# Kernel tuning notes

Hardware: AMD Instinct MI355X
Metric: run time of the kernel (lower is better)

The kernel has to match this reference:

```python
import jax, jax.numpy as jnp
import numpy as np

DIM = 128
CODEBOOK_SIZE = 1024


def setup_inputs() -> dict:
    key = jax.random.key(0)
    kx, ke = jax.random.split(key)
    x = jax.random.normal(kx, (16, 4096, DIM), dtype=jnp.float32)
    # kaiming_uniform_ on (codebook_size, dim): bound = sqrt(6 / fan_in), fan_in = dim
    bound = float(np.sqrt(6.0 / DIM))
    embed = jax.random.uniform(ke, (CODEBOOK_SIZE, DIM), dtype=jnp.float32,
                               minval=-bound, maxval=bound)
    return {"x": x, "embed": embed}


def reference(x, embed):
    orig_shape = x.shape
    flat = x.reshape(-1, x.shape[-1])                     # [N, D]
    x2 = jnp.sum(flat * flat, axis=1, keepdims=True)      # [N, 1]
    e2 = jnp.sum(embed * embed, axis=1)                   # [K]
    dist = -(x2 - 2.0 * (flat @ embed.T) + e2[None, :])   # [N, K]
    embed_ind = jnp.argmax(dist, axis=-1)                 # [N]
    embed_ind = embed_ind.reshape(orig_shape[:-1])        # [B, S]
    quantize = jnp.take(embed, embed_ind, axis=0)         # [B, S, D]
    return quantize, embed_ind
```

## Files before the change

### kernel.cpp

```cpp
#include <hip/hip_runtime.h>

#define DIM     128
#define NCODES  1024
#define TILE_M  64
#define BSTR    272
#define FLAGThr 0.018f
#define RPB     4
#define RGRID   1024

typedef __attribute__((ext_vector_type(8))) _Float16 half8;
typedef __attribute__((ext_vector_type(4))) _Float16 half4;
typedef __attribute__((ext_vector_type(4))) float    f32x4;


__global__ __launch_bounds__(256) void setup_kernel(
    const float* __restrict__ embed, double* __restrict__ e2d,
    float* __restrict__ e2f, _Float16* __restrict__ eh,
    float* __restrict__ embedT, int* __restrict__ cnt)
{
  __shared__ float tile[64][132];
  __shared__ double psum[4][64];
  if (blockIdx.x == 0 && threadIdx.x == 0) *cnt = 0;
  const int c0 = blockIdx.x * 64;
  const int t  = threadIdx.x;

  const f32x4* E4 = (const f32x4*)(embed + (size_t)c0 * DIM);
  #pragma unroll
  for (int i = 0; i < 8; ++i) {
    int e = t + i * 256;
    int r = e >> 5, c4 = e & 31;
    f32x4 v = E4[e];
    *(f32x4*)&tile[r][c4 * 4] = v;
    half4 h;
    h[0] = (_Float16)v[0]; h[1] = (_Float16)v[1];
    h[2] = (_Float16)v[2]; h[3] = (_Float16)v[3];
    *(half4*)&eh[(size_t)(c0 + r) * DIM + c4 * 4] = h;
  }
  __syncthreads();

  {
    int r = t & 63, part = t >> 6;
    double s = 0.0;
    #pragma unroll
    for (int k = 0; k < 32; ++k) {
      float v = tile[r][part * 32 + k];
      s += (double)v * v;
    }
    psum[part][r] = s;
  }
  __syncthreads();
  if (t < 64) {
    double s = psum[0][t] + psum[1][t] + psum[2][t] + psum[3][t];
    e2d[c0 + t] = s;
    e2f[c0 + t] = (float)s;
  }

  #pragma unroll
  for (int i = 0; i < 32; ++i) {
    int idx = t + i * 256;
    int k = idx >> 6, c = idx & 63;
    embedT[(size_t)k * NCODES + c0 + c] = tile[c][k];
  }
}

__global__ __launch_bounds__(256, 2) void pass1_kernel(
    const float* __restrict__ x, const float* __restrict__ embed,
    const _Float16* __restrict__ eh, const float* __restrict__ e2f,
    float* __restrict__ outQ, float* __restrict__ outIdx,
    int* __restrict__ cnt, int* __restrict__ list)
{
  __shared__ __align__(16) unsigned char lds[256 * BSTR];
  __shared__ float rb_best[4][TILE_M];
  __shared__ float rb_sec [4][TILE_M];
  __shared__ int   fidx[TILE_M];

  const int tid  = threadIdx.x;
  const int row0 = blockIdx.x * TILE_M;
  _Float16* xh = (_Float16*)lds;

  {
    const f32x4* x4 = (const f32x4*)(x + (size_t)row0 * DIM);
    #pragma unroll
    for (int i = 0; i < 8; ++i) {
      int e = tid + i * 256;
      int r = e >> 5, c4 = e & 31;
      f32x4 v = x4[e];
      half4 h;
      h[0] = (_Float16)v[0]; h[1] = (_Float16)v[1];
      h[2] = (_Float16)v[2]; h[3] = (_Float16)v[3];
      *(half4*)&xh[r * 136 + c4 * 4] = h;
    }
  }
  __syncthreads();

  const int l  = tid & 63, w = tid >> 6;
  const int rl = l & 15,  q = l >> 4;
  const int col0 = q * 8;

  half8 afrag[4][4];
  #pragma unroll
  for (int m = 0; m < 4; ++m)
    #pragma unroll
    for (int ks = 0; ks < 4; ++ks)
      afrag[m][ks] = *(const half8*)&xh[(m * 16 + rl) * 136 + ks * 32 + col0];

  float bestp[16], secp[16];
  #pragma unroll
  for (int s = 0; s < 16; ++s) { bestp[s] = -3.0e38f; secp[s] = -3.3e38f; }

  f32x4 t0[16];
  {
    const f32x4* src = (const f32x4*)eh;
    #pragma unroll
    for (int i = 0; i < 16; ++i) t0[i] = src[tid + i * 256];
  }
  __syncthreads();

  #pragma unroll
  for (int st = 0; st < 4; ++st) {
    #pragma unroll
    for (int i = 0; i < 16; ++i) {
      int e = tid + i * 256;
      *(f32x4*)&lds[(e >> 4) * BSTR + (e & 15) * 16] = t0[i];
    }
    f32x4 t1[16];
    if (st < 3) {
      const f32x4* src = (const f32x4*)(eh + (size_t)(st + 1) * 256 * DIM);
      #pragma unroll
      for (int i = 0; i < 16; ++i) t1[i] = src[tid + i * 256];
    }
    float vinit[4];
    #pragma unroll
    for (int sub = 0; sub < 4; ++sub)
      vinit[sub] = fmaf(-0.5f, e2f[st * 256 + w * 64 + sub * 16 + rl], -16.0f);

    __syncthreads();

    #pragma unroll
    for (int sub = 0; sub < 4; ++sub) {
      const int codeL  = w * 64 + sub * 16 + rl;
      const int mycode = st * 256 + codeL;
      half8 bfrag[4];
      #pragma unroll
      for (int ks = 0; ks < 4; ++ks)
        bfrag[ks] = *(const half8*)&lds[codeL * BSTR + ks * 64 + q * 16];
      f32x4 acc[4];
      #pragma unroll
      for (int m = 0; m < 4; ++m)
        acc[m] = (f32x4){vinit[sub], vinit[sub], vinit[sub], vinit[sub]};
      #pragma unroll
      for (int ks = 0; ks < 4; ++ks)
        #pragma unroll
        for (int m = 0; m < 4; ++m)
          acc[m] = __builtin_amdgcn_mfma_f32_16x16x32_f16(afrag[m][ks], bfrag[ks], acc[m], 0, 0, 0);
      #pragma unroll
      for (int m = 0; m < 4; ++m)
        #pragma unroll
        for (int r = 0; r < 4; ++r) {
          const int s = m * 4 + r;
          float scp = __int_as_float((__float_as_int(acc[m][r]) & ~1023) | mycode);
          secp[s]  = __builtin_amdgcn_fmed3f(scp, bestp[s], secp[s]);
          bestp[s] = fmaxf(bestp[s], scp);
        }
    }
    if (st < 3) {
      __syncthreads();
      #pragma unroll
      for (int i = 0; i < 16; ++i) t0[i] = t1[i];
    }
  }

  #pragma unroll
  for (int off = 1; off < 16; off <<= 1) {
    #pragma unroll
    for (int s = 0; s < 16; ++s) {
      float ob = __shfl_xor(bestp[s], off, 16);
      float os = __shfl_xor(secp[s],  off, 16);
      secp[s]  = fmaxf(__builtin_amdgcn_fmed3f(bestp[s], ob, secp[s]), os);
      bestp[s] = fmaxf(bestp[s], ob);
    }
  }
  if (rl == 0) {
    #pragma unroll
    for (int m = 0; m < 4; ++m)
      #pragma unroll
      for (int r = 0; r < 4; ++r) {
        int s = m * 4 + r;
        int row = m * 16 + q * 4 + r;
        rb_best[w][row] = bestp[s];
        rb_sec [w][row] = secp[s];
      }
  }
  __syncthreads();

  if (tid < TILE_M) {
    float bv = rb_best[0][tid], sv = rb_sec[0][tid];
    #pragma unroll
    for (int ww = 1; ww < 4; ++ww) {
      float ob = rb_best[ww][tid], os = rb_sec[ww][tid];
      sv = fmaxf(__builtin_amdgcn_fmed3f(bv, ob, sv), os);
      bv = fmaxf(bv, ob);
    }
    int bi = __float_as_int(bv) & 1023;
    int grow = row0 + tid;
    outIdx[grow] = (float)bi;
    fidx[tid] = bi;
    if (bv - sv <= FLAGThr) {
      int p = atomicAdd(cnt, 1);
      list[p] = grow;
    }
  }
  __syncthreads();

  {
    const f32x4* E4   = (const f32x4*)embed;
    f32x4*       out4 = (f32x4*)(outQ + (size_t)row0 * DIM);
    #pragma unroll
    for (int i = 0; i < 8; ++i) {
      int e = tid + i * 256;
      int r = e >> 5, c4 = e & 31;
      out4[e] = E4[fidx[r] * 32 + c4];
    }
  }
}

__global__ __launch_bounds__(256) void refine2_kernel(
    const float* __restrict__ x, const float* __restrict__ embed,
    const float* __restrict__ embedT,
    const double* __restrict__ e2d, const float* __restrict__ e2f,
    float* __restrict__ outQ, float* __restrict__ outIdx,
    const int* __restrict__ cnt, const int* __restrict__ list)
{
  __shared__ f32x4 xst[DIM];
  __shared__ float rb1[RPB][4], rb2[RPB][4];
  __shared__ int   ri1[RPB][4], ri2[RPB][4];
  __shared__ int   cand[RPB][2];

  const int t = threadIdx.x;
  const int l = t & 63, w = t >> 6;
  const int n = *cnt;
  float* xsf = (float*)xst;

  for (int base = blockIdx.x * RPB; base < n; base += RGRID * RPB) {
    const int nr = min(RPB, n - base);
    #pragma unroll
    for (int i = 0; i < 2; ++i) {
      int idx = t + i * 256;
      int r = idx >> 7, k = idx & 127;
      float v = 0.f;
      if (r < nr) v = x[(size_t)list[base + r] * DIM + k];
      xsf[k * RPB + r] = v;
    }
    __syncthreads();

    f32x4 dot[RPB];
    #pragma unroll
    for (int r = 0; r < RPB; ++r) dot[r] = (f32x4){0.f, 0.f, 0.f, 0.f};
    const f32x4* eT4 = (const f32x4*)embedT;
    #pragma unroll 4
    for (int k = 0; k < DIM; ++k) {
      f32x4 e4  = eT4[k * 256 + t];
      f32x4 xk4 = xst[k];
      #pragma unroll
      for (int r = 0; r < RPB; ++r) {
        dot[r][0] = fmaf(xk4[r], e4[0], dot[r][0]);
        dot[r][1] = fmaf(xk4[r], e4[1], dot[r][1]);
        dot[r][2] = fmaf(xk4[r], e4[2], dot[r][2]);
        dot[r][3] = fmaf(xk4[r], e4[3], dot[r][3]);
      }
    }

    #pragma unroll
    for (int r = 0; r < RPB; ++r) {
      float b1 = 3.4e38f, b2 = 3.4e38f; int i1 = 0, i2 = 0;
      #pragma unroll
      for (int j = 0; j < 4; ++j) {
        int c = 4 * t + j;
        float sc = fmaf(-2.0f, dot[r][j], e2f[c]);
        bool better = (sc < b1);
        float lv = better ? b1 : sc;  int li = better ? i1 : c;
        if (better) { b1 = sc; i1 = c; }
        bool t2 = (lv < b2) || (lv == b2 && li < i2);
        if (t2) { b2 = lv; i2 = li; }
      }
      #pragma unroll
      for (int off = 1; off < 64; off <<= 1) {
        float o1 = __shfl_xor(b1, off, 64); int oi1 = __shfl_xor(i1, off, 64);
        float o2 = __shfl_xor(b2, off, 64); int oi2 = __shfl_xor(i2, off, 64);
        bool take = (o1 < b1) || (o1 == b1 && oi1 < i1);
        float n1 = take ? o1 : b1; int ni1 = take ? oi1 : i1;
        float lo = take ? b1 : o1; int loi = take ? i1 : oi1;
        float c2v = take ? o2 : b2; int c2i = take ? oi2 : i2;
        bool u2 = (c2v < lo) || (c2v == lo && c2i < loi);
        b1 = n1; i1 = ni1;
        b2 = u2 ? c2v : lo; i2 = u2 ? c2i : loi;
      }
      if (l == 0) { rb1[r][w] = b1; ri1[r][w] = i1; rb2[r][w] = b2; ri2[r][w] = i2; }
    }
    __syncthreads();

    if (t < RPB) {
      float v1 = rb1[t][0], v2 = rb2[t][0]; int j1 = ri1[t][0], j2 = ri2[t][0];
      #pragma unroll
      for (int ww = 1; ww < 4; ++ww) {
        float o1 = rb1[t][ww], o2 = rb2[t][ww]; int oi1 = ri1[t][ww], oi2 = ri2[t][ww];
        bool take = (o1 < v1) || (o1 == v1 && oi1 < j1);
        float n1 = take ? o1 : v1; int ni1 = take ? oi1 : j1;
        float lo = take ? v1 : o1; int loi = take ? j1 : oi1;
        float c2v = take ? o2 : v2; int c2i = take ? oi2 : j2;
        bool u2 = (c2v < lo) || (c2v == lo && c2i < loi);
        v1 = n1; j1 = ni1; v2 = u2 ? c2v : lo; j2 = u2 ? c2i : loi;
      }
      cand[t][0] = j1; cand[t][1] = j2;
    }
    __syncthreads();

    if (w < nr) {
      int c1 = cand[w][0], c2 = cand[w][1];
      float xa = xsf[l * RPB + w], xb = xsf[(l + 64) * RPB + w];
      double p1 = (double)xa * (double)embed[(size_t)c1 * DIM + l]
                + (double)xb * (double)embed[(size_t)c1 * DIM + 64 + l];
      double p2 = (double)xa * (double)embed[(size_t)c2 * DIM + l]
                + (double)xb * (double)embed[(size_t)c2 * DIM + 64 + l];
      #pragma unroll
      for (int off = 1; off < 64; off <<= 1) {
        p1 += __shfl_xor(p1, off, 64);
        p2 += __shfl_xor(p2, off, 64);
      }
      double s1 = e2d[c1] - 2.0 * p1;
      double s2 = e2d[c2] - 2.0 * p2;
      int widx = ((s2 < s1) || (s2 == s1 && c2 < c1)) ? c2 : c1;
      int row = list[base + w];
      if (l == 0) outIdx[row] = (float)widx;
      outQ[(size_t)row * DIM + l]      = embed[(size_t)widx * DIM + l];
      outQ[(size_t)row * DIM + 64 + l] = embed[(size_t)widx * DIM + 64 + l];
    }
    __syncthreads();
  }
}

extern "C" void kernel_launch(void* const* d_in, const int* in_sizes, int n_in,
                              void* d_out, int out_size, void* d_ws, size_t ws_size,
                              hipStream_t stream) {
  const float* x     = (const float*)d_in[0];
  const float* embed = (const float*)d_in[1];
  const int N = in_sizes[0] / DIM;

  float* out    = (float*)d_out;
  float* outQ   = out;
  float* outIdx = out + (size_t)N * DIM;

  char* ws = (char*)d_ws;
  double*   e2d  = (double*)  (ws);
  float*    e2f  = (float*)   (ws + 8192);
  _Float16* eh   = (_Float16*)(ws + 12288);
  float*    eT   = (float*)   (ws + 274432);
  int*      cnt  = (int*)     (ws + 798720);
  int*      list = (int*)     (ws + 798976);

  setup_kernel  <<<NCODES / 64, 256, 0, stream>>>(embed, e2d, e2f, eh, eT, cnt);
  pass1_kernel  <<<N / TILE_M,  256, 0, stream>>>(x, embed, eh, e2f, outQ, outIdx, cnt, list);
  refine2_kernel<<<RGRID,       256, 0, stream>>>(x, embed, eT, e2d, e2f, outQ, outIdx, cnt, list);
}
```

Measured before the change: 141.9 us.

## Load codebook fragments directly from global memory instead of staging through LDS

Each wave now owns a contiguous 256-code slice and reads its half-precision codebook B fragments straight from global memory (L2/L1 cached), replacing the block-wide LDS staging of 256-code chunks, its register double-buffering and the barriers. Shared memory shrinks to the x tile, and launch bounds move from 2 to 4 blocks per CU to raise occupancy. The cost is more global/L2 traffic, since every block re-reads the whole fp16 codebook, and less latency hiding per wave because loads are no longer software-pipelined. The per-wave reduction across codes changes because each wave now covers different codes, but the cross-wave merge that follows is assumed to handle that.

Result: slower. 182.7 us (+28.7%).

```diff
diff --git a/kernel.cpp b/kernel.cpp
--- a/kernel.cpp
+++ b/kernel.cpp
@@ -3,7 +3,6 @@
 #define DIM     128
 #define NCODES  1024
 #define TILE_M  64
-#define BSTR    272
 #define FLAGThr 0.018f
 #define RPB     4
 #define RGRID   1024
@@ -63,20 +62,19 @@
   }
 }
 
-__global__ __launch_bounds__(256, 2) void pass1_kernel(
+__global__ __launch_bounds__(256, 4) void pass1_kernel(
     const float* __restrict__ x, const float* __restrict__ embed,
     const _Float16* __restrict__ eh, const float* __restrict__ e2f,
     float* __restrict__ outQ, float* __restrict__ outIdx,
     int* __restrict__ cnt, int* __restrict__ list)
 {
-  __shared__ __align__(16) unsigned char lds[256 * BSTR];
+  __shared__ __align__(16) _Float16 xh[TILE_M * 136];
   __shared__ float rb_best[4][TILE_M];
   __shared__ float rb_sec [4][TILE_M];
   __shared__ int   fidx[TILE_M];
 
   const int tid  = threadIdx.x;
   const int row0 = blockIdx.x * TILE_M;
-  _Float16* xh = (_Float16*)lds;
 
   {
     const f32x4* x4 = (const f32x4*)(x + (size_t)row0 * DIM);
@@ -95,78 +93,42 @@
 
   const int l  = tid & 63, w = tid >> 6;
   const int rl = l & 15,  q = l >> 4;
-  const int col0 = q * 8;
 
   half8 afrag[4][4];
   #pragma unroll
   for (int m = 0; m < 4; ++m)
     #pragma unroll
     for (int ks = 0; ks < 4; ++ks)
-      afrag[m][ks] = *(const half8*)&xh[(m * 16 + rl) * 136 + ks * 32 + col0];
+      afrag[m][ks] = *(const half8*)&xh[(m * 16 + rl) * 136 + ks * 32 + q * 8];
 
   float bestp[16], secp[16];
   #pragma unroll
   for (int s = 0; s < 16; ++s) { bestp[s] = -3.0e38f; secp[s] = -3.3e38f; }
 
-  f32x4 t0[16];
-  {
-    const f32x4* src = (const f32x4*)eh;
-    #pragma unroll
-    for (int i = 0; i < 16; ++i) t0[i] = src[tid + i * 256];
-  }
-  __syncthreads();
-
-  #pragma unroll
-  for (int st = 0; st < 4; ++st) {
-    #pragma unroll
-    for (int i = 0; i < 16; ++i) {
-      int e = tid + i * 256;
-      *(f32x4*)&lds[(e >> 4) * BSTR + (e & 15) * 16] = t0[i];
-    }
-    f32x4 t1[16];
-    if (st < 3) {
-      const f32x4* src = (const f32x4*)(eh + (size_t)(st + 1) * 256 * DIM);
-      #pragma unroll
-      for (int i = 0; i < 16; ++i) t1[i] = src[tid + i * 256];
-    }
-    float vinit[4];
-    #pragma unroll
-    for (int sub = 0; sub < 4; ++sub)
-      vinit[sub] = fmaf(-0.5f, e2f[st * 256 + w * 64 + sub * 16 + rl], -16.0f);
-
-    __syncthreads();
-
-    #pragma unroll
-    for (int sub = 0; sub < 4; ++sub) {
-      const int codeL  = w * 64 + sub * 16 + rl;
-      const int mycode = st * 256 + codeL;
-      half8 bfrag[4];
+  const _Float16* __restrict__ ehw = eh + ((size_t)w * 256 + rl) * DIM + q * 8;
+  const float*    __restrict__ e2w = e2f + w * 256 + rl;
+
+  #pragma unroll
+  for (int g = 0; g < 16; ++g) {
+    half8 bf[4];
+    #pragma unroll
+    for (int ks = 0; ks < 4; ++ks)
+      bf[ks] = *(const half8*)(ehw + (size_t)g * 16 * DIM + ks * 32);
+    const float vinit = fmaf(-0.5f, e2w[g * 16], -16.0f);
+    const int mycode = w * 256 + g * 16 + rl;
+    #pragma unroll
+    for (int m = 0; m < 4; ++m) {
+      f32x4 acc = (f32x4){vinit, vinit, vinit, vinit};
       #pragma unroll
       for (int ks = 0; ks < 4; ++ks)
-        bfrag[ks] = *(const half8*)&lds[codeL * BSTR + ks * 64 + q * 16];
-      f32x4 acc[4];
-      #pragma unroll
-      for (int m = 0; m < 4; ++m)
-        acc[m] = (f32x4){vinit[sub], vinit[sub], vinit[sub], vinit[sub]};
-      #pragma unroll
-      for (int ks = 0; ks < 4; ++ks)
-        #pragma unroll
-        for (int m = 0; m < 4; ++m)
-          acc[m] = __builtin_amdgcn_mfma_f32_16x16x32_f16(afrag[m][ks], bfrag[ks], acc[m], 0, 0, 0);
-      #pragma unroll
-      for (int m = 0; m < 4; ++m)
-        #pragma unroll
-        for (int r = 0; r < 4; ++r) {
-          const int s = m * 4 + r;
-          float scp = __int_as_float((__float_as_int(acc[m][r]) & ~1023) | mycode);
-          secp[s]  = __builtin_amdgcn_fmed3f(scp, bestp[s], secp[s]);
-          bestp[s] = fmaxf(bestp[s], scp);
-        }
-    }
-    if (st < 3) {
-      __syncthreads();
-      #pragma unroll
-      for (int i = 0; i < 16; ++i) t0[i] = t1[i];
+        acc = __builtin_amdgcn_mfma_f32_16x16x32_f16(afrag[m][ks], bf[ks], acc, 0, 0, 0);
+      #pragma unroll
+      for (int r = 0; r < 4; ++r) {
+        const int s = m * 4 + r;
+        float scp = __int_as_float((__float_as_int(acc[r]) & ~1023) | mycode);
+        secp[s]  = __builtin_amdgcn_fmed3f(scp, bestp[s], secp[s]);
+        bestp[s] = fmaxf(bestp[s], scp);
+      }
     }
   }
 
```
